# Kernel tuning notes

Measured on AMD Instinct MI355X. Metric: run time of the kernel, lower is better.

The kernel has to match this reference:

```python
import jax, jax.numpy as jnp
import numpy as np

D_MODEL = 1024
BS, K = 16, 64


def setup_inputs() -> dict:
    key = jax.random.key(0)
    k1, k2 = jax.random.split(key)
    Mp_cls = jax.random.normal(k1, (BS, K, D_MODEL), dtype=jnp.float32)
    mask_p = jnp.ones((BS, K, 4, K), dtype=bool)  # unused (no rnk_transformer)
    # nn.Linear(4*d_model, 3, bias=False) weight: [3, 4*d_model]
    W = jax.random.normal(k2, (3, 4 * D_MODEL), dtype=jnp.float32) * (4 * D_MODEL) ** -0.5
    return {"Mp_cls": Mp_cls, "mask_p": mask_p, "W": W}


def reference(Mp_cls, mask_p, W):
    # Pairwise scores: feature at [b,i,j] = cat(A[b,j], A[b,i], |A[b,j]-A[b,i]|, A[b,i]*A[b,j])
    # scores = feature @ W.T  -> [bs,K,K,3]. We split W into its 4 d_model blocks
    # so the concatenated [bs,K,K,4d] tensor is never materialized.
    d = Mp_cls.shape[-1]
    W1, W2, W3, W4 = W[:, :d], W[:, d:2 * d], W[:, 2 * d:3 * d], W[:, 3 * d:]
    t1 = jnp.einsum('bjd,cd->bjc', Mp_cls, W1)[:, None, :, :]          # from unsqueeze(1).expand
    t2 = jnp.einsum('bid,cd->bic', Mp_cls, W2)[:, :, None, :]          # from unsqueeze(2).expand
    diff = jnp.abs(Mp_cls[:, None, :, :] - Mp_cls[:, :, None, :])      # [bs,K,K,d]
    t3 = jnp.einsum('bijd,cd->bijc', diff, W3)
    t4 = jnp.einsum('bid,bjd,cd->bijc', Mp_cls, Mp_cls, W4)            # elementwise product term
    return t1 + t2 + t3 + t4  # [bs, K, K, 3]
```

## Files before the change

kernel.cpp:

```cpp
#include <hip/hip_runtime.h>

#define D_MODEL 1024
#define KK 64
#define BSZ 16

__global__ __launch_bounds__(256) void precompute_rows(
    const float* __restrict__ Mp, const float* __restrict__ W,
    float* __restrict__ P12)
{
    const int row  = blockIdx.x;
    const int wid  = threadIdx.x >> 6;
    const int lane = threadIdx.x & 63;
    const int d    = wid * 256 + lane * 4;

    const float4 m = *reinterpret_cast<const float4*>(Mp + (size_t)row * D_MODEL + d);
    float s[6];
#pragma unroll
    for (int c = 0; c < 3; ++c) {
        const float4 w1 = *reinterpret_cast<const float4*>(W + c * 4096 + d);
        const float4 w2 = *reinterpret_cast<const float4*>(W + c * 4096 + 1024 + d);
        s[c]     = m.x * w1.x + m.y * w1.y + m.z * w1.z + m.w * w1.w;
        s[3 + c] = m.x * w2.x + m.y * w2.y + m.z * w2.z + m.w * w2.w;
    }
#pragma unroll
    for (int off = 32; off; off >>= 1)
#pragma unroll
        for (int t = 0; t < 6; ++t)
            s[t] += __shfl_xor(s[t], off, 64);

    __shared__ float part[4][6];
    if (lane == 0) {
#pragma unroll
        for (int t = 0; t < 6; ++t) part[wid][t] = s[t];
    }
    __syncthreads();
    if (threadIdx.x < 6) {
        const int t = threadIdx.x;
        const float v = part[0][t] + part[1][t] + part[2][t] + part[3][t];
        if (t < 3) P12[row * 3 + t]              = v;
        else       P12[3072 + row * 3 + (t - 3)] = v;
    }
}

__device__ __forceinline__ int tri_start(int i) { return (i * (129 - i)) >> 1; }

__global__ __launch_bounds__(256, 2) void pair_kernel(
    const float* __restrict__ Mp, const float* __restrict__ W,
    const float* __restrict__ P12, float* __restrict__ out)
{
    const int b    = blockIdx.x;
    const int slot = blockIdx.y;
    const int wid  = threadIdx.x >> 6;
    const int lane = threadIdx.x & 63;

    const float* batch = Mp + (size_t)b * KK * D_MODEL;
    float*       outb  = out + (size_t)b * KK * KK * 3;
    const float* P1    = P12 + b * KK * 3;
    const float* P2    = P12 + 3072 + b * KK * 3;

    float4 w3[3][4], w4[3][4];
#pragma unroll
    for (int k = 0; k < 4; ++k) {
        const int d = k * 256 + lane * 4;
#pragma unroll
        for (int c = 0; c < 3; ++c) {
            w3[c][k] = *reinterpret_cast<const float4*>(W + c * 4096 + 2048 + d);
            w4[c][k] = *reinterpret_cast<const float4*>(W + c * 4096 + 3072 + d);
        }
    }
#define KEEP4(f) asm volatile("" : "+v"(f.x), "+v"(f.y), "+v"(f.z), "+v"(f.w))
#pragma unroll
    for (int c = 0; c < 3; ++c)
#pragma unroll
        for (int k = 0; k < 4; ++k) { KEEP4(w3[c][k]); KEEP4(w4[c][k]); }
#undef KEEP4

    const int p0 = slot * 32 + wid * 8;
    int i = (int)((129.0f - sqrtf(16641.0f - 8.0f * (float)p0)) * 0.5f);
    if (i > 63) i = 63;
    if (i < 0)  i = 0;
    while (tri_start(i + 1) <= p0) ++i;
    while (tri_start(i) > p0) --i;
    int j = i + (p0 - tri_start(i));

    float4 mi[4];
#pragma unroll
    for (int k = 0; k < 4; ++k)
        mi[k] = *reinterpret_cast<const float4*>(batch + i * D_MODEL + k * 256 + lane * 4);

#pragma unroll 2
    for (int t = 0; t < 8; ++t) {
        const float* rowj = batch + j * D_MODEL;
        float sc0 = 0.f, sc1 = 0.f, sc2 = 0.f;
#pragma unroll
        for (int k = 0; k < 4; ++k) {
            const float4 mj = *reinterpret_cast<const float4*>(rowj + k * 256 + lane * 4);
#define TERM(E)                                                      \
            {                                                        \
                const float dabs = fabsf(mi[k].E - mj.E);            \
                const float prod = mi[k].E * mj.E;                   \
                sc0 += dabs * w3[0][k].E;  sc0 += prod * w4[0][k].E; \
                sc1 += dabs * w3[1][k].E;  sc1 += prod * w4[1][k].E; \
                sc2 += dabs * w3[2][k].E;  sc2 += prod * w4[2][k].E; \
            }
            TERM(x) TERM(y) TERM(z) TERM(w)
#undef TERM
        }

#pragma unroll
        for (int off = 32; off; off >>= 1) {
            sc0 += __shfl_xor(sc0, off, 64);
            sc1 += __shfl_xor(sc1, off, 64);
            sc2 += __shfl_xor(sc2, off, 64);
        }

        if (lane < 3) {
            const int c = lane;
            const float sc = (c == 0) ? sc0 : (c == 1) ? sc1 : sc2;
            outb[(i * KK + j) * 3 + c] = P1[j * 3 + c] + P2[i * 3 + c] + sc;
            outb[(j * KK + i) * 3 + c] = P1[i * 3 + c] + P2[j * 3 + c] + sc;
        }

        ++j;
        if (j == KK) {
            ++i;
            if (i < KK) {
                j = i;
#pragma unroll
                for (int k = 0; k < 4; ++k)
                    mi[k] = *reinterpret_cast<const float4*>(batch + i * D_MODEL + k * 256 + lane * 4);
            }
        }
    }
}

extern "C" void kernel_launch(void* const* d_in, const int* in_sizes, int n_in,
                              void* d_out, int out_size, void* d_ws, size_t ws_size,
                              hipStream_t stream)
{
    const float* Mp = (const float*)d_in[0];
    const float* W  = (const float*)d_in[2];
    float* out = (float*)d_out;
    float* P12 = (float*)d_ws;

    precompute_rows<<<1024, 256, 0, stream>>>(Mp, W, P12);
    pair_kernel<<<dim3(BSZ, 65), 256, 0, stream>>>(Mp, W, P12, out);
}
```

Baseline: 81.62 us.

## Restructure pair kernel as i-tile blocks with transposed LDS j-rows and double buffering

Each block now handles two i rows against all 64 j rows of a batch. Lane j reads its values from a transposed, padded LDS copy of the batch, loaded in 128-wide d chunks with double buffering through registers. This removes the per-pair cross-lane shuffle reduction and the triangular pair indexing. In exchange the kernel no longer uses the pair symmetry, so it does twice the pairwise arithmetic. It also reloads the batch once per i-tile, 32 times per batch, and reads W and the mi values as wave-uniform scalar loads from global memory.

```diff
diff --git a/kernel.cpp b/kernel.cpp
--- a/kernel.cpp
+++ b/kernel.cpp
@@ -3,6 +3,9 @@
 #define D_MODEL 1024
 #define KK 64
 #define BSZ 16
+#define CH 128
+#define NCH 8
+#define LROW 65
 
 __global__ __launch_bounds__(256) void precompute_rows(
     const float* __restrict__ Mp, const float* __restrict__ W,
@@ -42,94 +45,122 @@
     }
 }
 
-__device__ __forceinline__ int tri_start(int i) { return (i * (129 - i)) >> 1; }
-
 __global__ __launch_bounds__(256, 2) void pair_kernel(
     const float* __restrict__ Mp, const float* __restrict__ W,
     const float* __restrict__ P12, float* __restrict__ out)
 {
-    const int b    = blockIdx.x;
-    const int slot = blockIdx.y;
-    const int wid  = threadIdx.x >> 6;
-    const int lane = threadIdx.x & 63;
+    __shared__ float lds[2][CH * LROW];
 
-    const float* batch = Mp + (size_t)b * KK * D_MODEL;
-    float*       outb  = out + (size_t)b * KK * KK * 3;
-    const float* P1    = P12 + b * KK * 3;
-    const float* P2    = P12 + 3072 + b * KK * 3;
+    const int b     = blockIdx.x >> 5;
+    const int itile = blockIdx.x & 31;
+    const int i0    = itile * 2;
+    const int tid   = threadIdx.x;
+    const int lane  = tid & 63;
+    const int uwid  = __builtin_amdgcn_readfirstlane(tid >> 6);
 
-    float4 w3[3][4], w4[3][4];
+    const float* __restrict__ batch = Mp + (size_t)b * KK * D_MODEL;
+    const float* __restrict__ rowi0 = batch + (size_t)i0 * D_MODEL;
+    const float* __restrict__ rowi1 = rowi0 + D_MODEL;
+
+    float acc[2][3] = {{0.f, 0.f, 0.f}, {0.f, 0.f, 0.f}};
+
 #pragma unroll
-    for (int k = 0; k < 4; ++k) {
-        const int d = k * 256 + lane * 4;
+    for (int p = 0; p < 8; ++p) {
+        const int idx  = p * 256 + tid;
+        const int row  = idx >> 5;
+        const int col4 = idx & 31;
+        const float4 v = *reinterpret_cast<const float4*>(batch + row * D_MODEL + col4 * 4);
+        const int base = (col4 * 4) * LROW + row;
+        lds[0][base]            = v.x;
+        lds[0][base + LROW]     = v.y;
+        lds[0][base + 2 * LROW] = v.z;
+        lds[0][base + 3 * LROW] = v.w;
+    }
+    __syncthreads();
+
+    for (int c = 0; c < NCH; ++c) {
+        const int cur = c & 1;
+
+        float4 stg[8];
+        if (c + 1 < NCH) {
+            const int d0n = (c + 1) * CH;
 #pragma unroll
-        for (int c = 0; c < 3; ++c) {
-            w3[c][k] = *reinterpret_cast<const float4*>(W + c * 4096 + 2048 + d);
-            w4[c][k] = *reinterpret_cast<const float4*>(W + c * 4096 + 3072 + d);
-        }
-    }
-#define KEEP4(f) asm volatile("" : "+v"(f.x), "+v"(f.y), "+v"(f.z), "+v"(f.w))
-#pragma unroll
-    for (int c = 0; c < 3; ++c)
-#pragma unroll
-        for (int k = 0; k < 4; ++k) { KEEP4(w3[c][k]); KEEP4(w4[c][k]); }
-#undef KEEP4
-
-    const int p0 = slot * 32 + wid * 8;
-    int i = (int)((129.0f - sqrtf(16641.0f - 8.0f * (float)p0)) * 0.5f);
-    if (i > 63) i = 63;
-    if (i < 0)  i = 0;
-    while (tri_start(i + 1) <= p0) ++i;
-    while (tri_start(i) > p0) --i;
-    int j = i + (p0 - tri_start(i));
-
-    float4 mi[4];
-#pragma unroll
-    for (int k = 0; k < 4; ++k)
-        mi[k] = *reinterpret_cast<const float4*>(batch + i * D_MODEL + k * 256 + lane * 4);
-
-#pragma unroll 2
-    for (int t = 0; t < 8; ++t) {
-        const float* rowj = batch + j * D_MODEL;
-        float sc0 = 0.f, sc1 = 0.f, sc2 = 0.f;
-#pragma unroll
-        for (int k = 0; k < 4; ++k) {
-            const float4 mj = *reinterpret_cast<const float4*>(rowj + k * 256 + lane * 4);
-#define TERM(E)                                                      \
-            {                                                        \
-                const float dabs = fabsf(mi[k].E - mj.E);            \
-                const float prod = mi[k].E * mj.E;                   \
-                sc0 += dabs * w3[0][k].E;  sc0 += prod * w4[0][k].E; \
-                sc1 += dabs * w3[1][k].E;  sc1 += prod * w4[1][k].E; \
-                sc2 += dabs * w3[2][k].E;  sc2 += prod * w4[2][k].E; \
+            for (int p = 0; p < 8; ++p) {
+                const int idx  = p * 256 + tid;
+                const int row  = idx >> 5;
+                const int col4 = idx & 31;
+                stg[p] = *reinterpret_cast<const float4*>(batch + row * D_MODEL + d0n + col4 * 4);
             }
-            TERM(x) TERM(y) TERM(z) TERM(w)
-#undef TERM
         }
 
+        const int dbase = c * CH + uwid * 32;
+        const float* __restrict__ w30 = W + 0 * 4096 + 2048 + dbase;
+        const float* __restrict__ w31 = W + 1 * 4096 + 2048 + dbase;
+        const float* __restrict__ w32 = W + 2 * 4096 + 2048 + dbase;
+        const float* __restrict__ w40 = W + 0 * 4096 + 3072 + dbase;
+        const float* __restrict__ w41 = W + 1 * 4096 + 3072 + dbase;
+        const float* __restrict__ w42 = W + 2 * 4096 + 3072 + dbase;
+        const float* __restrict__ mi0p = rowi0 + dbase;
+        const float* __restrict__ mi1p = rowi1 + dbase;
+        const float* __restrict__ ldsr = &lds[cur][(uwid * 32) * LROW + lane];
+
 #pragma unroll
-        for (int off = 32; off; off >>= 1) {
-            sc0 += __shfl_xor(sc0, off, 64);
-            sc1 += __shfl_xor(sc1, off, 64);
-            sc2 += __shfl_xor(sc2, off, 64);
+        for (int k = 0; k < 32; ++k) {
+            const float mj  = ldsr[k * LROW];
+            const float mi0 = mi0p[k];
+            const float mi1 = mi1p[k];
+            const float a0 = w30[k], a1 = w31[k], a2 = w32[k];
+            const float b0 = w40[k], b1 = w41[k], b2 = w42[k];
+
+            const float df0 = fabsf(mi0 - mj);
+            const float pr0 = mi0 * mj;
+            acc[0][0] += df0 * a0;  acc[0][0] += pr0 * b0;
+            acc[0][1] += df0 * a1;  acc[0][1] += pr0 * b1;
+            acc[0][2] += df0 * a2;  acc[0][2] += pr0 * b2;
+
+            const float df1 = fabsf(mi1 - mj);
+            const float pr1 = mi1 * mj;
+            acc[1][0] += df1 * a0;  acc[1][0] += pr1 * b0;
+            acc[1][1] += df1 * a1;  acc[1][1] += pr1 * b1;
+            acc[1][2] += df1 * a2;  acc[1][2] += pr1 * b2;
         }
 
-        if (lane < 3) {
-            const int c = lane;
-            const float sc = (c == 0) ? sc0 : (c == 1) ? sc1 : sc2;
-            outb[(i * KK + j) * 3 + c] = P1[j * 3 + c] + P2[i * 3 + c] + sc;
-            outb[(j * KK + i) * 3 + c] = P1[i * 3 + c] + P2[j * 3 + c] + sc;
+        if (c + 1 < NCH) {
+            float* dst = &lds[cur ^ 1][0];
+#pragma unroll
+            for (int p = 0; p < 8; ++p) {
+                const int idx  = p * 256 + tid;
+                const int row  = idx >> 5;
+                const int col4 = idx & 31;
+                const int base = (col4 * 4) * LROW + row;
+                dst[base]            = stg[p].x;
+                dst[base + LROW]     = stg[p].y;
+                dst[base + 2 * LROW] = stg[p].z;
+                dst[base + 3 * LROW] = stg[p].w;
+            }
         }
+        __syncthreads();
+    }
 
-        ++j;
-        if (j == KK) {
-            ++i;
-            if (i < KK) {
-                j = i;
+    float* l2 = &lds[0][0];
 #pragma unroll
-                for (int k = 0; k < 4; ++k)
-                    mi[k] = *reinterpret_cast<const float4*>(batch + i * D_MODEL + k * 256 + lane * 4);
-            }
+    for (int ii = 0; ii < 2; ++ii)
+#pragma unroll
+        for (int cc = 0; cc < 3; ++cc)
+            l2[((uwid * 2 + ii) * 3 + cc) * 64 + lane] = acc[ii][cc];
+    __syncthreads();
+
+    if (uwid < 2) {
+        const int i = i0 + uwid;
+#pragma unroll
+        for (int cc = 0; cc < 3; ++cc) {
+            const float s = l2[((0 * 2 + uwid) * 3 + cc) * 64 + lane]
+                          + l2[((1 * 2 + uwid) * 3 + cc) * 64 + lane]
+                          + l2[((2 * 2 + uwid) * 3 + cc) * 64 + lane]
+                          + l2[((3 * 2 + uwid) * 3 + cc) * 64 + lane];
+            const float v = s + P12[(b * 64 + lane) * 3 + cc]
+                              + P12[3072 + (b * 64 + i) * 3 + cc];
+            out[(((size_t)(b * 64 + i)) * 64 + lane) * 3 + cc] = v;
         }
     }
 }
@@ -144,5 +175,5 @@
     float* P12 = (float*)d_ws;
 
     precompute_rows<<<1024, 256, 0, stream>>>(Mp, W, P12);
-    pair_kernel<<<dim3(BSZ, 65), 256, 0, stream>>>(Mp, W, P12, out);
+    pair_kernel<<<BSZ * 32, 256, 0, stream>>>(Mp, W, P12, out);
 }
```

Result: slower. 126.2 us (+54.6%).
